# Kernel tuning notes

Hardware: AMD Instinct MI355X
Metric: run time of the kernel (lower is better)

## Reference

```python
import jax, jax.numpy as jnp
import numpy as np

EPS = 1e-5

def _conv_bn_relu(x, w, gamma, beta):
    # x: [B, C, N], w: [O, C] (1x1 conv, no bias)
    y = jnp.einsum('oc,bcn->bon', w, x)
    # BatchNorm1d in training mode: per-channel stats over (B, N)
    mean = jnp.mean(y, axis=(0, 2), keepdims=True)
    var = jnp.var(y, axis=(0, 2), keepdims=True)
    yhat = (y - mean) * jax.lax.rsqrt(var + EPS)
    return jax.nn.relu(gamma[None, :, None] * yhat + beta[None, :, None])


def setup_inputs() -> dict:
    key = jax.random.key(0)
    ks = jax.random.split(key, 8)
    B, C, N, Cr = 4, 256, 4096, 32
    x = jax.random.normal(ks[0], (B, C, N), dtype=jnp.float32)
    w1 = jax.random.normal(ks[1], (Cr, C), dtype=jnp.float32) * (1.0 / np.sqrt(C))
    w2 = jax.random.normal(ks[2], (Cr, C), dtype=jnp.float32) * (1.0 / np.sqrt(C))
    w3 = jax.random.normal(ks[3], (C, C), dtype=jnp.float32) * (1.0 / np.sqrt(C))
    g1 = 1.0 + 0.1 * jax.random.normal(ks[4], (Cr,), dtype=jnp.float32)
    b1 = 0.1 * jax.random.normal(ks[5], (Cr,), dtype=jnp.float32)
    g2 = 1.0 + 0.1 * jax.random.normal(ks[6], (Cr,), dtype=jnp.float32)
    b2 = 0.1 * jax.random.normal(ks[7], (Cr,), dtype=jnp.float32)
    g3 = jnp.ones((C,), dtype=jnp.float32)
    b3 = jnp.zeros((C,), dtype=jnp.float32)
    return {'x': x, 'w1': w1, 'w2': w2, 'w3': w3,
            'g1': g1, 'b1': b1, 'g2': g2, 'b2': b2, 'g3': g3, 'b3': b3}


def reference(x, w1, w2, w3, g1, b1, g2, b2, g3, b3):
    # a: [B, N, Cr] (queries), k: [B, Cr, N] (keys)
    a = _conv_bn_relu(x, w1, g1, b1).transpose(0, 2, 1)
    k = _conv_bn_relu(x, w2, g2, b2)
    # s[b, n, m] = softmax_m(sum_c a[b,n,c] * k[b,c,m])
    s = jax.nn.softmax(jnp.einsum('bnc,bcm->bnm', a, k), axis=-1)
    d = _conv_bn_relu(x, w3, g3, b3)  # [B, C, N]
    # out = x + d @ s^T : out[b,c,m] = sum_n d[b,c,n] * s[m,n]
    out = x + jnp.einsum('bcn,bmn->bcm', d, s)
    return out
```

## Files before the change

### kernel.cpp

```cpp
#include <hip/hip_runtime.h>
#include <cstddef>
#include <cstdint>

#define B_ 4
#define C_ 256
#define N_ 4096
#define KF_OFF_B  ((size_t)1024 * 1024)
#define DF_OFF_B  ((size_t)2 * 1024 * 1024)
#define SUM_OFF_B ((size_t)10 * 1024 * 1024)
#define ML_OFF_B  (SUM_OFF_B + 1280 * 4)
#define XH_OFF_B  (ML_OFF_B + 524288)
#define XL_OFF_B  (XH_OFF_B + (size_t)8 * 1024 * 1024)
#define WH_OFF_B  (XL_OFF_B + (size_t)8 * 1024 * 1024)
#define WL_OFF_B  (WH_OFF_B + 163840)
#define LOG2E 1.4426950408889634f

typedef unsigned short bfraw;
typedef __attribute__((ext_vector_type(8))) short short8;
typedef __attribute__((ext_vector_type(4))) float float4v;
typedef __attribute__((ext_vector_type(4))) bfraw bfraw4;

__device__ inline bfraw f2bf(float f) {
    union { float f; uint32_t u; } c; c.f = f;
    uint32_t u = c.u;
    u += 0x7fffu + ((u >> 16) & 1u);
    return (bfraw)(u >> 16);
}
__device__ inline float bf2f(bfraw h) {
    union { uint32_t u; float f; } c; c.u = ((uint32_t)h) << 16;
    return c.f;
}
#if __has_builtin(__builtin_amdgcn_exp2f)
__device__ inline float EXP2(float x) { return __builtin_amdgcn_exp2f(x); }
#else
__device__ inline float EXP2(float x) { return exp2f(x); }
#endif
__device__ inline uint32_t pack2(float a, float b) {
    union { float f; uint32_t u; } ca, cb; ca.f = a; cb.f = b;
#if __has_builtin(__builtin_amdgcn_perm)
    return __builtin_amdgcn_perm(cb.u + 0x8000u, ca.u + 0x8000u, 0x07060302u);
#else
    return ((ca.u + 0x8000u) >> 16) | ((cb.u + 0x8000u) & 0xffff0000u);
#endif
}

__global__ __launch_bounds__(256) void prep_kernel(
    const float* __restrict__ x,
    const float* __restrict__ w1, const float* __restrict__ w2,
    const float* __restrict__ w3, uint8_t* __restrict__ wsb)
{
    __shared__ float Ls[64][65];
    if (blockIdx.x >= 1024) {
        int bid = blockIdx.x - 1024;
        if (bid == 0) {
            float* sums = (float*)(wsb + SUM_OFF_B);
            for (int i = threadIdx.x; i < 640; i += 256) sums[i] = 0.f;
        }
        bfraw* wh = (bfraw*)(wsb + WH_OFF_B);
        bfraw* wl = (bfraw*)(wsb + WL_OFF_B);
        int idx4 = (bid * 256 + threadIdx.x) * 4;
        int ch = idx4 >> 8, k = idx4 & 255;
        const float* wr = (ch < 32) ? (w1 + ch * C_)
                          : (ch < 64) ? (w2 + (ch - 32) * C_)
                                      : (w3 + (ch - 64) * C_);
        float4 v = *(const float4*)&wr[k];
        float va[4] = {v.x, v.y, v.z, v.w};
        bfraw4 h, l;
#pragma unroll
        for (int j = 0; j < 4; ++j) {
            h[j] = f2bf(va[j]);
            l[j] = f2bf(va[j] - bf2f(h[j]));
        }
        *(bfraw4*)&wh[idx4] = h;
        *(bfraw4*)&wl[idx4] = l;
        return;
    }
    bfraw* xh = (bfraw*)(wsb + XH_OFF_B);
    bfraw* xl = (bfraw*)(wsb + XL_OFF_B);
    const int id = blockIdx.x;
    const int b  = id >> 8;
    const int c0 = ((id >> 6) & 3) << 6;
    const int n0 = (id & 63) << 6;
    const int t  = threadIdx.x;
    {
        int cl = t >> 4, nc = (t & 15) << 2;
#pragma unroll
        for (int i = 0; i < 4; ++i) {
            float4 v = *(const float4*)&x[((size_t)b * C_ + c0 + cl + i * 16) * N_ + n0 + nc];
            Ls[cl + i * 16][nc + 0] = v.x;
            Ls[cl + i * 16][nc + 1] = v.y;
            Ls[cl + i * 16][nc + 2] = v.z;
            Ls[cl + i * 16][nc + 3] = v.w;
        }
    }
    __syncthreads();
    int nl = t >> 2, seg = t & 3;
    bfraw hb[16], lb[16];
#pragma unroll
    for (int j = 0; j < 16; ++j) {
        float v = Ls[seg * 16 + j][nl];
        bfraw h = f2bf(v);
        hb[j] = h;
        lb[j] = f2bf(v - bf2f(h));
    }
    size_t base = ((size_t)b * N_ + n0 + nl) * 256 + c0 + seg * 16;
    *(short8*)&xh[base]     = *(short8*)&hb[0];
    *(short8*)&xh[base + 8] = *(short8*)&hb[8];
    *(short8*)&xl[base]     = *(short8*)&lb[0];
    *(short8*)&xl[base + 8] = *(short8*)&lb[8];
}

__global__ __launch_bounds__(256, 2) void ygemm_kernel(uint8_t* __restrict__ wsb)
{
    const bfraw* xh = (const bfraw*)(wsb + XH_OFF_B);
    const bfraw* xl = (const bfraw*)(wsb + XL_OFF_B);
    const bfraw* wh = (const bfraw*)(wsb + WH_OFF_B);
    const bfraw* wl = (const bfraw*)(wsb + WL_OFF_B);
    bfraw* qf  = (bfraw*)wsb;
    bfraw* kfp = (bfraw*)(wsb + KF_OFF_B);
    bfraw* dfp = (bfraw*)(wsb + DF_OFF_B);
    float* sums  = (float*)(wsb + SUM_OFF_B);
    float* sumsq = sums + 320;
    __shared__ float redS[4][64], redQ[4][64];

    const int bx = blockIdx.x;
    const int by = blockIdx.y;
    const int b  = bx >> 5;
    const int n0 = (bx << 7) & (N_ - 1);
    const int t = threadIdx.x, w = t >> 6, l = t & 63, lq = l & 15, lg = l >> 4;
    const int nw = n0 + w * 32;

    float4v acc[4][2];
#pragma unroll
    for (int i = 0; i < 4; ++i)
#pragma unroll
        for (int j = 0; j < 2; ++j) acc[i][j] = (float4v){0.f, 0.f, 0.f, 0.f};

    for (int s = 0; s < 8; ++s) {
        const int k0 = s * 32;
        short8 ah[4], al[4], bh[2], bl[2];
#pragma unroll
        for (int ct = 0; ct < 4; ++ct) {
            size_t off = (size_t)(by * 64 + ct * 16 + lq) * 256 + k0 + lg * 8;
            ah[ct] = *(const short8*)&wh[off];
            al[ct] = *(const short8*)&wl[off];
        }
#pragma unroll
        for (int nt = 0; nt < 2; ++nt) {
            size_t off = ((size_t)b * N_ + nw + nt * 16 + lq) * 256 + k0 + lg * 8;
            bh[nt] = *(const short8*)&xh[off];
            bl[nt] = *(const short8*)&xl[off];
        }
#pragma unroll
        for (int ct = 0; ct < 4; ++ct)
#pragma unroll
            for (int nt = 0; nt < 2; ++nt) {
                acc[ct][nt] = __builtin_amdgcn_mfma_f32_16x16x32_bf16(ah[ct], bh[nt], acc[ct][nt], 0, 0, 0);
                acc[ct][nt] = __builtin_amdgcn_mfma_f32_16x16x32_bf16(al[ct], bh[nt], acc[ct][nt], 0, 0, 0);
                acc[ct][nt] = __builtin_amdgcn_mfma_f32_16x16x32_bf16(ah[ct], bl[nt], acc[ct][nt], 0, 0, 0);
            }
    }
#pragma unroll
    for (int ct = 0; ct < 4; ++ct) {
        float sv[4], qv[4];
#pragma unroll
        for (int r = 0; r < 4; ++r) {
            float a0 = acc[ct][0][r], a1 = acc[ct][1][r];
            sv[r] = a0 + a1;
            qv[r] = a0 * a0 + a1 * a1;
#pragma unroll
            for (int m = 1; m < 16; m <<= 1) {
                sv[r] += __shfl_xor(sv[r], m);
                qv[r] += __shfl_xor(qv[r], m);
            }
        }
        if (lq == 0) {
#pragma unroll
            for (int r = 0; r < 4; ++r) {
                redS[w][ct * 16 + lg * 4 + r] = sv[r];
                redQ[w][ct * 16 + lg * 4 + r] = qv[r];
            }
        }
    }
    __syncthreads();
    if (t < 64) {
        float s = redS[0][t] + redS[1][t] + redS[2][t] + redS[3][t];
        float q = redQ[0][t] + redQ[1][t] + redQ[2][t] + redQ[3][t];
        atomicAdd(&sums[by * 64 + t], s);
        atomicAdd(&sumsq[by * 64 + t], q);
    }
    if (by == 0) {
#pragma unroll
        for (int ct = 0; ct < 4; ++ct)
#pragma unroll
            for (int nt = 0; nt < 2; ++nt)
#pragma unroll
                for (int r = 0; r < 4; ++r) {
                    int c = ct * 16 + lg * 4 + r;
                    int n = nw + nt * 16 + lq;
                    size_t addr = ((size_t)(b << 8) + (n >> 4)) * 512
                                + (size_t)(((n & 15) | (((c >> 3) & 3) << 4)) << 3) + (c & 7);
                    bfraw v = f2bf(acc[ct][nt][r]);
                    if (c < 32) qf[addr] = v; else kfp[addr] = v;
                }
    } else {
#pragma unroll
        for (int ct = 0; ct < 4; ++ct)
#pragma unroll
            for (int nt = 0; nt < 2; ++nt)
#pragma unroll
                for (int r = 0; r < 4; ++r) {
                    int cg = (by - 1) * 64 + ct * 16 + lg * 4 + r;
                    int n = nw + nt * 16 + lq;
                    size_t addr = (((size_t)(b << 4) + (cg >> 4)) * 128 + (n >> 5)) * 512
                                + (size_t)(((cg & 15) | (((n >> 3) & 3) << 4)) << 3) + (n & 7);
                    dfp[addr] = f2bf(acc[ct][nt][r]);
                }
    }
}

__device__ inline void bn_coef(const float* __restrict__ sums,
                               const float* __restrict__ g1, const float* __restrict__ b1,
                               const float* __restrict__ g2, const float* __restrict__ b2,
                               const float* __restrict__ g3, const float* __restrict__ b3,
                               int ch, float& sc, float& bi)
{
    const float inv = 1.0f / (float)(B_ * N_);
    float mean = sums[ch] * inv;
    float var  = sums[320 + ch] * inv - mean * mean;
    float g, bb;
    if (ch < 32)      { g = g1[ch];      bb = b1[ch]; }
    else if (ch < 64) { g = g2[ch - 32]; bb = b2[ch - 32]; }
    else              { g = g3[ch - 64]; bb = b3[ch - 64]; }
    sc = g * rsqrtf(var + 1e-5f);
    bi = bb - sc * mean;
    if (ch < 32) { sc *= LOG2E; bi *= LOG2E; }
}

__global__ __launch_bounds__(256) void affine_kernel(
    uint8_t* __restrict__ wsb,
    const float* __restrict__ g1, const float* __restrict__ b1,
    const float* __restrict__ g2, const float* __restrict__ b2,
    const float* __restrict__ g3, const float* __restrict__ b3)
{
    bfraw* base = (bfraw*)wsb;
    const float* sums = (const float*)(wsb + SUM_OFF_B);
    size_t i8 = ((size_t)blockIdx.x * 256 + threadIdx.x) * 8;
    bfraw4 v0 = *(bfraw4*)&base[i8];
    bfraw4 v1 = *(bfraw4*)&base[i8 + 4];
    if (i8 < 1048576) {
        int ch0 = (((int)(i8 >> 7)) & 3) * 8 + ((i8 < 524288) ? 0 : 32);
        float sa[8], ca[8];
#pragma unroll
        for (int j = 0; j < 8; ++j)
            bn_coef(sums, g1, b1, g2, b2, g3, b3, ch0 + j, sa[j], ca[j]);
#pragma unroll
        for (int j = 0; j < 4; ++j) {
            v0[j] = f2bf(fmaxf(0.f, fmaf(sa[j],     bf2f(v0[j]), ca[j])));
            v1[j] = f2bf(fmaxf(0.f, fmaf(sa[j + 4], bf2f(v1[j]), ca[j + 4])));
        }
    } else {
        size_t rel = i8 - 1048576;
        int ch = 64 + (((int)(rel >> 16)) & 15) * 16 + (((int)(rel >> 3)) & 15);
        float s, b;
        bn_coef(sums, g1, b1, g2, b2, g3, b3, ch, s, b);
#pragma unroll
        for (int j = 0; j < 4; ++j) {
            v0[j] = f2bf(fmaxf(0.f, fmaf(s, bf2f(v0[j]), b)));
            v1[j] = f2bf(fmaxf(0.f, fmaf(s, bf2f(v1[j]), b)));
        }
    }
    *(bfraw4*)&base[i8] = v0;
    *(bfraw4*)&base[i8 + 4] = v1;
}

__global__ __launch_bounds__(256, 2) void flash_kernel(
    const float* __restrict__ x, const uint8_t* __restrict__ wsb,
    float* __restrict__ out)
{
    const bfraw* qf  = (const bfraw*)wsb;
    const bfraw* kfp = (const bfraw*)(wsb + KF_OFF_B);
    const bfraw* dfp = (const bfraw*)(wsb + DF_OFF_B);
    __shared__ bfraw Pl[2][32 * 256];
    __shared__ bfraw kst[2][16 * 512];
    __shared__ float lsh[2][32];

    const int id  = blockIdx.x;
    const int b   = id & 3;
    const int n0q = (id >> 2) << 5;
    const int tid = threadIdx.x;
    const int w   = tid >> 6;
    const int l   = tid & 63;
    const int lq  = l & 15;
    const int lg  = l >> 4;
    const int sw  = lq & 7;
    const int qt_s   = w >> 1;
    const int ks_loc = w & 1;

    const short8 qfrag = *(const short8*)&qf[((size_t)(b * 256 + (n0q >> 4) + qt_s)) * 512 + l * 8];
    const float4v zv = {-16.f, -16.f, -16.f, -16.f};

    float ps = 0.f;
    float4v acc[4][2];
#pragma unroll
    for (int i = 0; i < 4; ++i)
#pragma unroll
        for (int j = 0; j < 2; ++j) acc[i][j] = (float4v){0.f, 0.f, 0.f, 0.f};

    short8 dfr[4][4];
#pragma unroll
    for (int i = 0; i < 4; ++i)
#pragma unroll
        for (int c = 0; c < 4; ++c)
            dfr[i][c] = *(const short8*)&dfp[(((size_t)(b * 16 + w + 4 * i)) * 128 + c) * 512 + l * 8];
    {
#pragma unroll
        for (int j = 0; j < 4; ++j) {
            short8 v = *(const short8*)&kfp[((size_t)(b * 256 + 4 * w + j)) * 512 + l * 8];
            *(short8*)&kst[0][(4 * w + j) * 512 + l * 8] = v;
        }
    }
    __syncthreads();

    const int qrow = qt_s * 16 + lq;
    for (int it = 0; it < 16; ++it) {
        const int ib = it & 1;
        const int nit = (it + 1) & 15;
        short8 kstage[4];
#pragma unroll
        for (int j = 0; j < 4; ++j)
            kstage[j] = *(const short8*)&kfp[((size_t)(b * 256 + nit * 16 + 4 * w + j)) * 512 + l * 8];
        short8 kfr[8];
#pragma unroll
        for (int kt = 0; kt < 8; ++kt)
            kfr[kt] = *(const short8*)&kst[ib][(ks_loc * 8 + kt) * 512 + l * 8];
        float4v st[8];
#pragma unroll
        for (int kt = 0; kt < 8; ++kt)
            st[kt] = __builtin_amdgcn_mfma_f32_16x16x32_bf16(kfr[kt], qfrag, zv, 0, 0, 0);
#pragma unroll
        for (int kt = 0; kt < 8; ++kt) {
            float e0 = EXP2(st[kt][0]);
            float e1 = EXP2(st[kt][1]);
            float e2 = EXP2(st[kt][2]);
            float e3 = EXP2(st[kt][3]);
            ps += (e0 + e1) + (e2 + e3);
            uint2 pd = {pack2(e0, e1), pack2(e2, e3)};
            int g = (2 * (ks_loc * 8 + kt) + (lg >> 1)) ^ sw;
            *(uint2*)&Pl[ib][qrow * 256 + g * 8 + (lg & 1) * 4] = pd;
        }
#pragma unroll
        for (int j = 0; j < 4; ++j)
            *(short8*)&kst[ib ^ 1][(4 * w + j) * 512 + l * 8] = kstage[j];
        __syncthreads();
#pragma unroll
        for (int ch = 0; ch < 8; ++ch) {
            short8 bfr[2];
            int g = (ch * 4 + lg) ^ sw;
#pragma unroll
            for (int qt = 0; qt < 2; ++qt)
                bfr[qt] = *(const short8*)&Pl[ib][(qt * 16 + lq) * 256 + g * 8];
            __builtin_amdgcn_s_setprio(1);
#pragma unroll
            for (int i = 0; i < 4; ++i)
#pragma unroll
                for (int qt = 0; qt < 2; ++qt)
                    acc[i][qt] = __builtin_amdgcn_mfma_f32_16x16x32_bf16(dfr[i][ch & 3], bfr[qt], acc[i][qt], 0, 0, 0);
            __builtin_amdgcn_s_setprio(0);
            int rch = (ch < 4) ? (it * 8 + ch + 4) : (nit * 8 + ch - 4);
#pragma unroll
            for (int i = 0; i < 4; ++i)
                dfr[i][ch & 3] = *(const short8*)&dfp[(((size_t)(b * 16 + w + 4 * i)) * 128 + rch) * 512 + l * 8];
        }
    }
    ps += __shfl_xor(ps, 16);
    ps += __shfl_xor(ps, 32);
    if (lg == 0) lsh[ks_loc][qrow] = ps;
    __syncthreads();
    float inv[2];
#pragma unroll
    for (int qt = 0; qt < 2; ++qt)
        inv[qt] = 1.0f / (lsh[0][qt * 16 + lq] + lsh[1][qt * 16 + lq]);
#pragma unroll
    for (int i = 0; i < 4; ++i) {
        int ctg = w + 4 * i;
#pragma unroll
        for (int r = 0; r < 4; ++r) {
            int c = ctg * 16 + lg * 4 + r;
            size_t base = ((size_t)b * C_ + c) * N_ + n0q;
#pragma unroll
            for (int qt = 0; qt < 2; ++qt) {
                size_t idx = base + qt * 16 + lq;
                out[idx] = x[idx] + acc[i][qt][r] * inv[qt];
            }
        }
    }
}

extern "C" void kernel_launch(void* const* d_in, const int* in_sizes, int n_in,
                              void* d_out, int out_size, void* d_ws, size_t ws_size,
                              hipStream_t stream) {
    (void)in_sizes; (void)n_in; (void)out_size; (void)ws_size;
    const float* x  = (const float*)d_in[0];
    const float* w1 = (const float*)d_in[1];
    const float* w2 = (const float*)d_in[2];
    const float* w3 = (const float*)d_in[3];
    const float* g1 = (const float*)d_in[4];
    const float* b1 = (const float*)d_in[5];
    const float* g2 = (const float*)d_in[6];
    const float* b2 = (const float*)d_in[7];
    const float* g3 = (const float*)d_in[8];
    const float* b3 = (const float*)d_in[9];
    uint8_t* wsb = (uint8_t*)d_ws;
    float* outp = (float*)d_out;

    prep_kernel<<<1104, 256, 0, stream>>>(x, w1, w2, w3, wsb);
    ygemm_kernel<<<dim3(128, 5), 256, 0, stream>>>(wsb);
    affine_kernel<<<2560, 256, 0, stream>>>(wsb, g1, b1, g2, b2, g3, b3);
    flash_kernel<<<512, 256, 0, stream>>>(x, wsb, outp);
}
```

Before: 180.0 us.

## Double flash kernel query tile to 64 rows with 8 waves per block

Grows each flash block from 32 to 64 query rows and from 4 to 8 waves, halving the grid to 256 blocks. Each K tile staged in shared memory is now shared by twice as many queries, and each wave loads two K rows instead of four, cutting redundant global K traffic. Waves split by query pair and channel quarter, so every D fragment is now read by two waves per block. The cost is twice the shared memory for P, fewer blocks per GPU (256 blocks on a device with many CUs), and heavier per-block barrier synchronisation.

```diff
diff --git a/kernel.cpp b/kernel.cpp
--- a/kernel.cpp
+++ b/kernel.cpp
@@ -274,20 +274,20 @@
     *(bfraw4*)&base[i8 + 4] = v1;
 }
 
-__global__ __launch_bounds__(256, 2) void flash_kernel(
+__global__ __launch_bounds__(512, 2) void flash_kernel(
     const float* __restrict__ x, const uint8_t* __restrict__ wsb,
     float* __restrict__ out)
 {
     const bfraw* qf  = (const bfraw*)wsb;
     const bfraw* kfp = (const bfraw*)(wsb + KF_OFF_B);
     const bfraw* dfp = (const bfraw*)(wsb + DF_OFF_B);
-    __shared__ bfraw Pl[2][32 * 256];
+    __shared__ bfraw Pl[2][64 * 256];
     __shared__ bfraw kst[2][16 * 512];
-    __shared__ float lsh[2][32];
+    __shared__ float lsh[2][64];
 
     const int id  = blockIdx.x;
     const int b   = id & 3;
-    const int n0q = (id >> 2) << 5;
+    const int n0q = (id >> 2) << 6;
     const int tid = threadIdx.x;
     const int w   = tid >> 6;
     const int l   = tid & 63;
@@ -296,6 +296,8 @@
     const int sw  = lq & 7;
     const int qt_s   = w >> 1;
     const int ks_loc = w & 1;
+    const int qp  = w >> 2;
+    const int cq  = w & 3;
 
     const short8 qfrag = *(const short8*)&qf[((size_t)(b * 256 + (n0q >> 4) + qt_s)) * 512 + l * 8];
     const float4v zv = {-16.f, -16.f, -16.f, -16.f};
@@ -312,13 +314,12 @@
     for (int i = 0; i < 4; ++i)
 #pragma unroll
         for (int c = 0; c < 4; ++c)
-            dfr[i][c] = *(const short8*)&dfp[(((size_t)(b * 16 + w + 4 * i)) * 128 + c) * 512 + l * 8];
+            dfr[i][c] = *(const short8*)&dfp[(((size_t)(b * 16 + cq + 4 * i)) * 128 + c) * 512 + l * 8];
     {
-#pragma unroll
-        for (int j = 0; j < 4; ++j) {
-            short8 v = *(const short8*)&kfp[((size_t)(b * 256 + 4 * w + j)) * 512 + l * 8];
-            *(short8*)&kst[0][(4 * w + j) * 512 + l * 8] = v;
-        }
+        short8 v0 = *(const short8*)&kfp[((size_t)(b * 256 + w)) * 512 + l * 8];
+        short8 v1 = *(const short8*)&kfp[((size_t)(b * 256 + w + 8)) * 512 + l * 8];
+        *(short8*)&kst[0][w * 512 + l * 8] = v0;
+        *(short8*)&kst[0][(w + 8) * 512 + l * 8] = v1;
     }
     __syncthreads();
 
@@ -326,10 +327,8 @@
     for (int it = 0; it < 16; ++it) {
         const int ib = it & 1;
         const int nit = (it + 1) & 15;
-        short8 kstage[4];
-#pragma unroll
-        for (int j = 0; j < 4; ++j)
-            kstage[j] = *(const short8*)&kfp[((size_t)(b * 256 + nit * 16 + 4 * w + j)) * 512 + l * 8];
+        short8 kstage0 = *(const short8*)&kfp[((size_t)(b * 256 + nit * 16 + w)) * 512 + l * 8];
+        short8 kstage1 = *(const short8*)&kfp[((size_t)(b * 256 + nit * 16 + w + 8)) * 512 + l * 8];
         short8 kfr[8];
 #pragma unroll
         for (int kt = 0; kt < 8; ++kt)
@@ -349,9 +348,8 @@
             int g = (2 * (ks_loc * 8 + kt) + (lg >> 1)) ^ sw;
             *(uint2*)&Pl[ib][qrow * 256 + g * 8 + (lg & 1) * 4] = pd;
         }
-#pragma unroll
-        for (int j = 0; j < 4; ++j)
-            *(short8*)&kst[ib ^ 1][(4 * w + j) * 512 + l * 8] = kstage[j];
+        *(short8*)&kst[ib ^ 1][w * 512 + l * 8] = kstage0;
+        *(short8*)&kst[ib ^ 1][(w + 8) * 512 + l * 8] = kstage1;
         __syncthreads();
 #pragma unroll
         for (int ch = 0; ch < 8; ++ch) {
@@ -359,7 +357,7 @@
             int g = (ch * 4 + lg) ^ sw;
 #pragma unroll
             for (int qt = 0; qt < 2; ++qt)
-                bfr[qt] = *(const short8*)&Pl[ib][(qt * 16 + lq) * 256 + g * 8];
+                bfr[qt] = *(const short8*)&Pl[ib][((2 * qp + qt) * 16 + lq) * 256 + g * 8];
             __builtin_amdgcn_s_setprio(1);
 #pragma unroll
             for (int i = 0; i < 4; ++i)
@@ -370,7 +368,7 @@
             int rch = (ch < 4) ? (it * 8 + ch + 4) : (nit * 8 + ch - 4);
 #pragma unroll
             for (int i = 0; i < 4; ++i)
-                dfr[i][ch & 3] = *(const short8*)&dfp[(((size_t)(b * 16 + w + 4 * i)) * 128 + rch) * 512 + l * 8];
+                dfr[i][ch & 3] = *(const short8*)&dfp[(((size_t)(b * 16 + cq + 4 * i)) * 128 + rch) * 512 + l * 8];
         }
     }
     ps += __shfl_xor(ps, 16);
@@ -379,18 +377,20 @@
     __syncthreads();
     float inv[2];
 #pragma unroll
-    for (int qt = 0; qt < 2; ++qt)
-        inv[qt] = 1.0f / (lsh[0][qt * 16 + lq] + lsh[1][qt * 16 + lq]);
+    for (int qt = 0; qt < 2; ++qt) {
+        int qg = (2 * qp + qt) * 16 + lq;
+        inv[qt] = 1.0f / (lsh[0][qg] + lsh[1][qg]);
+    }
 #pragma unroll
     for (int i = 0; i < 4; ++i) {
-        int ctg = w + 4 * i;
+        int ctg = cq + 4 * i;
 #pragma unroll
         for (int r = 0; r < 4; ++r) {
             int c = ctg * 16 + lg * 4 + r;
             size_t base = ((size_t)b * C_ + c) * N_ + n0q;
 #pragma unroll
             for (int qt = 0; qt < 2; ++qt) {
-                size_t idx = base + qt * 16 + lq;
+                size_t idx = base + (2 * qp + qt) * 16 + lq;
                 out[idx] = x[idx] + acc[i][qt][r] * inv[qt];
             }
         }
@@ -417,5 +417,5 @@
     prep_kernel<<<1104, 256, 0, stream>>>(x, w1, w2, w3, wsb);
     ygemm_kernel<<<dim3(128, 5), 256, 0, stream>>>(wsb);
     affine_kernel<<<2560, 256, 0, stream>>>(wsb, g1, b1, g2, b2, g3, b3);
-    flash_kernel<<<512, 256, 0, stream>>>(x, wsb, outp);
-}
+    flash_kernel<<<256, 512, 0, stream>>>(x, wsb, outp);
+}
```

Measured after the change: 184.2 us. 2.3% more time.
